# Kernel optimization log

Hardware: AMD Instinct MI355X
Metric: run time of the kernel (lower is better)

The kernel has to match this reference:

```python
import jax, jax.numpy as jnp
import numpy as np
import math

EMBED = 1024
N_HEAD = 16
T_LEN = 2048
BATCH = 2
MLP_MULT = 4
EPS = 1e-5


def setup_inputs() -> dict:
    key = jax.random.key(0)
    ks = jax.random.split(key, 12)
    d = EMBED
    h = MLP_MULT * d
    s = 0.02
    return {
        "x": jax.random.normal(ks[0], (BATCH, T_LEN, d), dtype=jnp.float32),
        "ln1_scale": jnp.ones((d,), jnp.float32),
        "ln1_shift": jnp.zeros((d,), jnp.float32),
        "w_qkv": jax.random.normal(ks[1], (d, 3 * d), jnp.float32) * s,
        "b_qkv": jnp.zeros((3 * d,), jnp.float32),
        "ln2_scale": jnp.ones((d,), jnp.float32),
        "ln2_shift": jnp.zeros((d,), jnp.float32),
        "w_fc": jax.random.normal(ks[2], (d, h), jnp.float32) * s,
        "b_fc": jnp.zeros((h,), jnp.float32),
        "w_proj": jax.random.normal(ks[3], (h, d), jnp.float32) * s,
        "b_proj": jnp.zeros((d,), jnp.float32),
    }


def _layer_norm(x, scale, shift):
    mu = jnp.mean(x, axis=-1, keepdims=True)
    var = jnp.var(x, axis=-1, keepdims=True)
    return (x - mu) * jax.lax.rsqrt(var + EPS) * scale + shift


def _attention(h, w_qkv, b_qkv):
    B, T, C = h.shape
    hd = C // N_HEAD
    qkv = h @ w_qkv + b_qkv  # [B,T,3C]
    q, k, v = jnp.split(qkv, 3, axis=-1)
    q = q.reshape(B, T, N_HEAD, hd)
    k = k.reshape(B, T, N_HEAD, hd)
    v = v.reshape(B, T, N_HEAD, hd)
    scores = jnp.einsum("bthd,bshd->bhts", q, k) * (1.0 / math.sqrt(hd))
    causal = jnp.tril(jnp.ones((T, T), dtype=bool))
    scores = jnp.where(causal[None, None], scores, -jnp.inf)
    probs = jax.nn.softmax(scores, axis=-1)
    y = jnp.einsum("bhts,bshd->bthd", probs, v)
    return y.reshape(B, T, C)


def reference(x, ln1_scale, ln1_shift, w_qkv, b_qkv, ln2_scale, ln2_shift,
              w_fc, b_fc, w_proj, b_proj):
    x = x + _attention(_layer_norm(x, ln1_scale, ln1_shift), w_qkv, b_qkv)
    h = _layer_norm(x, ln2_scale, ln2_shift)
    # note: module names it 'gelu' but it's nn.ReLU()
    h = jax.nn.relu(h @ w_fc + b_fc) @ w_proj + b_proj
    return x + h
```

## Files before the change

### kernel.cpp

```cpp
#include <hip/hip_runtime.h>
#include <hip/hip_bf16.h>


typedef __bf16  bf16x8  __attribute__((ext_vector_type(8)));
typedef __bf16  bf16x4  __attribute__((ext_vector_type(4)));
typedef float   floatx4 __attribute__((ext_vector_type(4)));

#define T_LEN 2048
#define EMB   1024
#define NH    16
#define HD    64
#define HID   4096

#define GLOBAL_LOAD_LDS16(gp, lp) \
    __builtin_amdgcn_global_load_lds( \
        (const __attribute__((address_space(1))) void*)(gp), \
        (__attribute__((address_space(3))) void*)(lp), 16, 0, 0)

__global__ void transpose_cast(const float* __restrict__ in,
                               __bf16* __restrict__ out, int R, int C) {
    __shared__ float tile[32][33];
    int bc = blockIdx.x * 32;
    int br = blockIdx.y * 32;
    int tx = threadIdx.x;
    int ty = threadIdx.y;
    for (int i = 0; i < 32; i += 8) {
        tile[ty + i][tx] = in[(size_t)(br + ty + i) * C + bc + tx];
    }
    __syncthreads();
    for (int i = 0; i < 32; i += 8) {
        int c = bc + ty + i, r = br + tx;
        out[(size_t)c * R + r] = (__bf16)tile[tx][ty + i];
    }
}

__global__ __launch_bounds__(256)
void ln_kernel(const float* __restrict__ in, const float* __restrict__ sc,
               const float* __restrict__ sh, __bf16* __restrict__ out) {
    int row = blockIdx.x;
    const float* p = in + (size_t)row * EMB;
    int tid = threadIdx.x;
    int lane = tid & 63, wave = tid >> 6;
    float v[4];
    float s = 0.f, s2 = 0.f;
    for (int j = 0; j < 4; j++) {
        v[j] = p[tid + j * 256];
        s += v[j]; s2 += v[j] * v[j];
    }
    for (int m = 1; m < 64; m <<= 1) {
        s  += __shfl_xor(s, m);
        s2 += __shfl_xor(s2, m);
    }
    __shared__ float ssum[4], ssum2[4];
    if (lane == 0) { ssum[wave] = s; ssum2[wave] = s2; }
    __syncthreads();
    float tot  = ssum[0] + ssum[1] + ssum[2] + ssum[3];
    float tot2 = ssum2[0] + ssum2[1] + ssum2[2] + ssum2[3];
    float mean = tot * (1.f / EMB);
    float var  = tot2 * (1.f / EMB) - mean * mean;
    float rstd = rsqrtf(var + 1e-5f);
    for (int j = 0; j < 4; j++) {
        int c = tid + j * 256;
        out[(size_t)row * EMB + c] = (__bf16)((v[j] - mean) * rstd * sc[c] + sh[c]);
    }
}

__global__ __launch_bounds__(512)
void gemm256(const __bf16* __restrict__ A, const __bf16* __restrict__ Bt,
             const float* __restrict__ bias, const float* __restrict__ res,
             float* __restrict__ outF, __bf16* __restrict__ outB,
             int M, int N, int lda, int KL, int relu, int gx, int gz) {
    __shared__ __align__(16) __bf16 sA[2][256][64];
    __shared__ __align__(16) __bf16 sB[2][256][64];
    const int BUFE = 256 * 64;
    int tid  = threadIdx.x;
    int lane = tid & 63, wave = tid >> 6;
    int quad = lane >> 4, l16 = lane & 15;

    int i  = blockIdx.x;
    int c  = i & 7, m = i >> 3;
    int bx = m % gx;
    int p  = (m / gx) * 8 + c;
    int by = p / gz;
    int bz = p - by * gz;

    int bm = by * 256, bn = bx * 256;
    size_t k0 = (size_t)bz * KL;
    int wm = (wave >> 2) * 128, wn = (wave & 3) * 64;

    floatx4 acc[8][4] = {};

    int srow  = tid >> 3;
    int sslot = (tid & 7) ^ (srow & 7);
    const __bf16* gA = A  + (size_t)(bm + srow) * lda + k0 + sslot * 8;
    const __bf16* gB = Bt + (size_t)(bn + srow) * lda + k0 + sslot * 8;
    __bf16* lA = &sA[0][0][0] + wave * 512;
    __bf16* lB = &sB[0][0][0] + wave * 512;
    const size_t rstep = (size_t)64 * lda;

#define STAGE256(nb, ko) do { \
    GLOBAL_LOAD_LDS16(gA + (ko),             lA + (nb) * BUFE); \
    GLOBAL_LOAD_LDS16(gB + (ko),             lB + (nb) * BUFE); \
    GLOBAL_LOAD_LDS16(gA + (ko) + rstep,     lA + (nb) * BUFE + 4096); \
    GLOBAL_LOAD_LDS16(gB + (ko) + rstep,     lB + (nb) * BUFE + 4096); \
    GLOBAL_LOAD_LDS16(gA + (ko) + 2 * rstep, lA + (nb) * BUFE + 8192); \
    GLOBAL_LOAD_LDS16(gB + (ko) + 2 * rstep, lB + (nb) * BUFE + 8192); \
    GLOBAL_LOAD_LDS16(gA + (ko) + 3 * rstep, lA + (nb) * BUFE + 12288); \
    GLOBAL_LOAD_LDS16(gB + (ko) + 3 * rstep, lB + (nb) * BUFE + 12288); \
} while (0)

    STAGE256(0, (size_t)0);

    int xs0  = ((quad) ^ (l16 & 7)) * 8;
    int xs1  = ((4 + quad) ^ (l16 & 7)) * 8;
    int aoff = (wm + l16) * 64;
    int boff = (wn + l16) * 64;

    const int nt = KL / 64;
    for (int t = 0; t < nt; ++t) {
        const int cur = t & 1;
        __builtin_amdgcn_s_barrier();
        asm volatile("" ::: "memory");
        if (t + 1 < nt) {
            STAGE256(cur ^ 1, (size_t)(t + 1) * 64);
            asm volatile("s_waitcnt vmcnt(8)" ::: "memory");
        } else {
            asm volatile("s_waitcnt vmcnt(0)" ::: "memory");
        }
        __builtin_amdgcn_s_barrier();
        asm volatile("" ::: "memory");
        __builtin_amdgcn_sched_barrier(0);

        const __bf16* sAc = &sA[0][0][0] + cur * BUFE;
        const __bf16* sBc = &sB[0][0][0] + cur * BUFE;

        bf16x8 a0[4][2], a1[4][2], b0[2][2], b1[2][2];

        #pragma unroll
        for (int mi = 0; mi < 4; ++mi) {
            a0[mi][0] = *(const bf16x8*)(sAc + aoff + mi * 1024 + xs0);
            a0[mi][1] = *(const bf16x8*)(sAc + aoff + mi * 1024 + xs1);
        }
        #pragma unroll
        for (int nj = 0; nj < 2; ++nj) {
            b0[nj][0] = *(const bf16x8*)(sBc + boff + nj * 1024 + xs0);
            b0[nj][1] = *(const bf16x8*)(sBc + boff + nj * 1024 + xs1);
        }
        __builtin_amdgcn_s_setprio(1);
        #pragma unroll
        for (int mi = 0; mi < 4; ++mi)
            #pragma unroll
            for (int nj = 0; nj < 2; ++nj) {
                acc[mi][nj] = __builtin_amdgcn_mfma_f32_16x16x32_bf16(
                    a0[mi][0], b0[nj][0], acc[mi][nj], 0, 0, 0);
                acc[mi][nj] = __builtin_amdgcn_mfma_f32_16x16x32_bf16(
                    a0[mi][1], b0[nj][1], acc[mi][nj], 0, 0, 0);
            }
        __builtin_amdgcn_s_setprio(0);

        #pragma unroll
        for (int nj = 0; nj < 2; ++nj) {
            b1[nj][0] = *(const bf16x8*)(sBc + boff + (2 + nj) * 1024 + xs0);
            b1[nj][1] = *(const bf16x8*)(sBc + boff + (2 + nj) * 1024 + xs1);
        }
        __builtin_amdgcn_s_setprio(1);
        #pragma unroll
        for (int mi = 0; mi < 4; ++mi)
            #pragma unroll
            for (int nj = 0; nj < 2; ++nj) {
                acc[mi][2 + nj] = __builtin_amdgcn_mfma_f32_16x16x32_bf16(
                    a0[mi][0], b1[nj][0], acc[mi][2 + nj], 0, 0, 0);
                acc[mi][2 + nj] = __builtin_amdgcn_mfma_f32_16x16x32_bf16(
                    a0[mi][1], b1[nj][1], acc[mi][2 + nj], 0, 0, 0);
            }
        __builtin_amdgcn_s_setprio(0);

        #pragma unroll
        for (int mi = 0; mi < 4; ++mi) {
            a1[mi][0] = *(const bf16x8*)(sAc + aoff + (4 + mi) * 1024 + xs0);
            a1[mi][1] = *(const bf16x8*)(sAc + aoff + (4 + mi) * 1024 + xs1);
        }
        __builtin_amdgcn_s_setprio(1);
        #pragma unroll
        for (int mi = 0; mi < 4; ++mi)
            #pragma unroll
            for (int nj = 0; nj < 2; ++nj) {
                acc[4 + mi][2 + nj] = __builtin_amdgcn_mfma_f32_16x16x32_bf16(
                    a1[mi][0], b1[nj][0], acc[4 + mi][2 + nj], 0, 0, 0);
                acc[4 + mi][2 + nj] = __builtin_amdgcn_mfma_f32_16x16x32_bf16(
                    a1[mi][1], b1[nj][1], acc[4 + mi][2 + nj], 0, 0, 0);
            }
        __builtin_amdgcn_s_setprio(0);

        __builtin_amdgcn_s_setprio(1);
        #pragma unroll
        for (int mi = 0; mi < 4; ++mi)
            #pragma unroll
            for (int nj = 0; nj < 2; ++nj) {
                acc[4 + mi][nj] = __builtin_amdgcn_mfma_f32_16x16x32_bf16(
                    a1[mi][0], b0[nj][0], acc[4 + mi][nj], 0, 0, 0);
                acc[4 + mi][nj] = __builtin_amdgcn_mfma_f32_16x16x32_bf16(
                    a1[mi][1], b0[nj][1], acc[4 + mi][nj], 0, 0, 0);
            }
        __builtin_amdgcn_s_setprio(0);
    }
#undef STAGE256

    if (bias) {
        #pragma unroll
        for (int mi = 0; mi < 8; ++mi) {
            int row0 = bm + wm + mi * 16 + quad * 4;
            #pragma unroll
            for (int nj = 0; nj < 4; ++nj) {
                int col = bn + wn + nj * 16 + l16;
                float bv = bias[col];
                #pragma unroll
                for (int r = 0; r < 4; ++r) {
                    size_t idx = (size_t)(row0 + r) * N + col;
                    float cc = acc[mi][nj][r] + bv;
                    if (relu) cc = fmaxf(cc, 0.f);
                    if (res)  cc += res[idx];
                    if (outF) outF[idx] = cc;
                    if (outB) outB[idx] = (__bf16)cc;
                }
            }
        }
    } else {
        __bf16* po = outB + (size_t)bz * M * N;
        #pragma unroll
        for (int mi = 0; mi < 8; ++mi) {
            int row0 = bm + wm + mi * 16 + quad * 4;
            #pragma unroll
            for (int nj = 0; nj < 4; ++nj) {
                int col = bn + wn + nj * 16 + l16;
                #pragma unroll
                for (int r = 0; r < 4; ++r)
                    po[(size_t)(row0 + r) * N + col] = (__bf16)acc[mi][nj][r];
            }
        }
    }
}

__global__ __launch_bounds__(256)
void reduce_proj(const __bf16* __restrict__ pbuf, const float* __restrict__ x2,
                 const float* __restrict__ bias, float* __restrict__ out) {
    const size_t MN = (size_t)4096 * 1024;
    size_t i = (size_t)blockIdx.x * 256 + threadIdx.x;
    float4 r = ((const float4*)x2)[i];
    float4 bb = ((const float4*)bias)[i & 255];
    float acc0 = r.x + bb.x, acc1 = r.y + bb.y;
    float acc2 = r.z + bb.z, acc3 = r.w + bb.w;
    for (int k = 0; k < 4; k++) {
        bf16x4 pv = *(const bf16x4*)&pbuf[k * MN + i * 4];
        acc0 += (float)pv[0]; acc1 += (float)pv[1];
        acc2 += (float)pv[2]; acc3 += (float)pv[3];
    }
    float4 o = {acc0, acc1, acc2, acc3};
    ((float4*)out)[i] = o;
}

__global__ __launch_bounds__(256)
void gemm_bt_n64(const __bf16* __restrict__ A, const __bf16* __restrict__ Bt,
                 const float* __restrict__ bias, const float* __restrict__ res,
                 float* __restrict__ outF, __bf16* __restrict__ outB,
                 int M, int N, int K, int relu) {
    __shared__ __align__(16) __bf16 sA[128][40];
    __shared__ __align__(16) __bf16 sB[64][40];
    int tid  = threadIdx.x;
    int lane = tid & 63, wave = tid >> 6;
    int quad = lane >> 4, l16 = lane & 15;
    int bm = blockIdx.y * 128, bn = blockIdx.x * 64;
    int wm = (wave & 1) * 64, wn = (wave >> 1) * 32;
    floatx4 acc[4][2] = {};

    int srow = tid >> 2;
    int scol = (tid & 3) * 8;
    const __bf16* gA = &A[(size_t)(bm + srow) * K + scol];
    const __bf16* gB = &Bt[(size_t)(bn + srow) * K + scol];

    uint4 ra0 = *(const uint4*)gA;
    uint4 ra1 = *(const uint4*)(gA + (size_t)64 * K);
    uint4 rb0 = *(const uint4*)gB;

    for (int kk = 0; kk < K; kk += 32) {
        __syncthreads();
        *(uint4*)&sA[srow][scol]      = ra0;
        *(uint4*)&sA[srow + 64][scol] = ra1;
        *(uint4*)&sB[srow][scol]      = rb0;
        __syncthreads();
        {
            int kn = (kk + 32 < K) ? kk + 32 : kk;
            ra0 = *(const uint4*)(gA + kn);
            ra1 = *(const uint4*)(gA + kn + (size_t)64 * K);
            rb0 = *(const uint4*)(gB + kn);
        }
        bf16x8 af[4], bfr[2];
        for (int i = 0; i < 4; i++)
            af[i] = *(const bf16x8*)&sA[wm + i * 16 + l16][quad * 8];
        for (int j = 0; j < 2; j++)
            bfr[j] = *(const bf16x8*)&sB[wn + j * 16 + l16][quad * 8];
        for (int i = 0; i < 4; i++)
            for (int j = 0; j < 2; j++)
                acc[i][j] = __builtin_amdgcn_mfma_f32_16x16x32_bf16(
                    af[i], bfr[j], acc[i][j], 0, 0, 0);
    }

    for (int i = 0; i < 4; i++) {
        int row0 = bm + wm + i * 16 + quad * 4;
        for (int j = 0; j < 2; j++) {
            int col = bn + wn + j * 16 + l16;
            float bv = bias[col];
            for (int r = 0; r < 4; r++) {
                size_t idx = (size_t)(row0 + r) * N + col;
                float c = acc[i][j][r] + bv;
                if (relu) c = fmaxf(c, 0.f);
                if (res)  c += res[idx];
                if (outF) outF[idx] = c;
                if (outB) outB[idx] = (__bf16)c;
            }
        }
    }
}

__global__ __launch_bounds__(256)
void attn_kernel(const __bf16* __restrict__ qkv, const float* __restrict__ x,
                 float* __restrict__ x2) {
    __shared__ __align__(16) __bf16 sK[2][64][72];
    __shared__ __align__(16) __bf16 sVt[2][64][72];
    __shared__ __align__(16) __bf16 sP[4][16][72];
    const int tid  = threadIdx.x;
    const int lane = tid & 63, wave = tid >> 6;
    const int quad = lane >> 4, l16 = lane & 15;

    int i = blockIdx.x;
    int c = i & 7, m = i >> 3;
    const int bh = (m & 3) * 8 + c;
    const int qb = 31 - (m >> 2);
    const int h  = bh & (NH - 1);
    const int b  = bh >> 4;
    const size_t rowbase = (size_t)b * T_LEN;
    const int qrow = qb * 64 + wave * 16;

    const float kQScale = 0.125f * 1.44269504088896f;
    bf16x8 ones;
    for (int j = 0; j < 8; j++) ones[j] = (__bf16)1.0f;

    const int key0 = tid >> 3, m8 = tid & 7;
    const int key1 = key0 + 32;
    const __bf16* kp0 = qkv + (rowbase + key0) * 3072 + h * HD + m8 * 8 + 1024;
    const __bf16* kp1 = qkv + (rowbase + key1) * 3072 + h * HD + m8 * 8 + 1024;
    const int pc0 = ((key0 >> 3) ^ m8) * 8 + (key0 & 7);
    const int pc1 = ((key1 >> 3) ^ m8) * 8 + (key1 & 7);

    bf16x8 qf[2];
    for (int ks = 0; ks < 2; ks++) {
        bf16x8 raw = *(const bf16x8*)&qkv[(rowbase + qrow + l16) * 3072
                                          + h * HD + ks * 32 + quad * 8];
        for (int j = 0; j < 8; j++)
            qf[ks][j] = (__bf16)((float)raw[j] * kQScale);
    }

    floatx4 o[4] = {}, ol = {};

    const int ntiles = qb + 1;
    const size_t TSTEP = (size_t)64 * 3072;

    uint4 kr0 = *(const uint4*)kp0;
    uint4 kr1 = *(const uint4*)kp1;
    uint4 vr0 = *(const uint4*)(kp0 + 1024);
    uint4 vr1 = *(const uint4*)(kp1 + 1024);
    {
        *(uint4*)&sK[0][key0][m8 * 8] = kr0;
        *(uint4*)&sK[0][key1][m8 * 8] = kr1;
        bf16x8 v0 = *(bf16x8*)&vr0, v1 = *(bf16x8*)&vr1;
        for (int j = 0; j < 8; j++) sVt[0][m8 * 8 + j][pc0] = v0[j];
        for (int j = 0; j < 8; j++) sVt[0][m8 * 8 + j][pc1] = v1[j];
    }
    {
        size_t o1 = (ntiles > 1) ? TSTEP : 0;
        kr0 = *(const uint4*)(kp0 + o1);
        kr1 = *(const uint4*)(kp1 + o1);
        vr0 = *(const uint4*)(kp0 + o1 + 1024);
        vr1 = *(const uint4*)(kp1 + o1 + 1024);
    }
    __syncthreads();

    for (int kt = 0; kt < ntiles; kt++) {
        const int cur = kt & 1, nxt = cur ^ 1;
        if (kt + 1 < ntiles) {
            *(uint4*)&sK[nxt][key0][m8 * 8] = kr0;
            *(uint4*)&sK[nxt][key1][m8 * 8] = kr1;
            bf16x8 v0 = *(bf16x8*)&vr0, v1 = *(bf16x8*)&vr1;
            for (int j = 0; j < 8; j++) sVt[nxt][m8 * 8 + j][pc0] = v0[j];
            for (int j = 0; j < 8; j++) sVt[nxt][m8 * 8 + j][pc1] = v1[j];
            size_t offn = (size_t)((kt + 2 < ntiles) ? kt + 2 : kt + 1) * TSTEP;
            kr0 = *(const uint4*)(kp0 + offn);
            kr1 = *(const uint4*)(kp1 + offn);
            vr0 = *(const uint4*)(kp0 + offn + 1024);
            vr1 = *(const uint4*)(kp1 + offn + 1024);
        }

        floatx4 s_acc[4] = {};
        for (int jt = 0; jt < 4; jt++)
            for (int ks = 0; ks < 2; ks++) {
                bf16x8 kf = *(const bf16x8*)&sK[cur][jt * 16 + l16]
                                              [ks * 32 + quad * 8];
                s_acc[jt] = __builtin_amdgcn_mfma_f32_16x16x32_bf16(
                    qf[ks], kf, s_acc[jt], 0, 0, 0);
            }

        if (kt == qb) {
            const int tq0 = qrow + quad * 4;
            const int k0 = kt * 64;
            for (int jt = 0; jt < 4; jt++) {
                int key = k0 + jt * 16 + l16;
                for (int r = 0; r < 4; r++) {
                    float sv = (key <= tq0 + r) ? s_acc[jt][r] : -1e30f;
                    float pv = __builtin_amdgcn_exp2f(fminf(sv, 30.f));
                    sP[wave][quad * 4 + r][jt * 16 + l16] = (__bf16)pv;
                }
            }
        } else {
            for (int jt = 0; jt < 4; jt++)
                for (int r = 0; r < 4; r++) {
                    float pv = __builtin_amdgcn_exp2f(fminf(s_acc[jt][r], 30.f));
                    sP[wave][quad * 4 + r][jt * 16 + l16] = (__bf16)pv;
                }
        }

        for (int kp = 0; kp < 2; kp++) {
            bf16x8 pf = *(const bf16x8*)&sP[wave][l16][kp * 32 + quad * 8];
            ol = __builtin_amdgcn_mfma_f32_16x16x32_bf16(pf, ones, ol, 0, 0, 0);
            for (int jt2 = 0; jt2 < 4; jt2++) {
                int d = jt2 * 16 + l16;
                int pg = (kp * 4 + quad) ^ (d >> 3);
                bf16x8 vf = *(const bf16x8*)&sVt[cur][d][pg * 8];
                o[jt2] = __builtin_amdgcn_mfma_f32_16x16x32_bf16(
                    pf, vf, o[jt2], 0, 0, 0);
            }
        }
        __syncthreads();
    }

    float inv[4];
    for (int r = 0; r < 4; r++) inv[r] = __builtin_amdgcn_rcpf(ol[r]);
    for (int jt2 = 0; jt2 < 4; jt2++) {
        for (int r = 0; r < 4; r++) {
            int tq  = qrow + quad * 4 + r;
            int col = h * HD + jt2 * 16 + l16;
            size_t gi = (rowbase + tq) * EMB + col;
            x2[gi] = x[gi] + o[jt2][r] * inv[r];
        }
    }
}

extern "C" void kernel_launch(void* const* d_in, const int* in_sizes, int n_in,
                              void* d_out, int out_size, void* d_ws, size_t ws_size,
                              hipStream_t stream) {
    const float* x      = (const float*)d_in[0];
    const float* ln1_s  = (const float*)d_in[1];
    const float* ln1_b  = (const float*)d_in[2];
    const float* w_qkv  = (const float*)d_in[3];
    const float* b_qkv  = (const float*)d_in[4];
    const float* ln2_s  = (const float*)d_in[5];
    const float* ln2_b  = (const float*)d_in[6];
    const float* w_fc   = (const float*)d_in[7];
    const float* b_fc   = (const float*)d_in[8];
    const float* w_proj = (const float*)d_in[9];
    const float* b_proj = (const float*)d_in[10];
    float* out = (float*)d_out;

    const int M = 2 * T_LEN;
    char* ws = (char*)d_ws;
    size_t off = 0;
    auto alloc = [&](size_t bytes) {
        void* p = ws + off; off += (bytes + 255) & ~(size_t)255; return p;
    };
    __bf16* wpj_t  = (__bf16*)alloc((size_t)1024 * 4096 * 2);
    float*  x2     = (float*) alloc((size_t)M * 1024 * 4);
    __bf16* hfc    = (__bf16*)alloc((size_t)M * 4096 * 2);
    size_t mark = off;
    __bf16* wqkv_t = (__bf16*)alloc((size_t)3072 * 1024 * 2);
    __bf16* wfc_t  = (__bf16*)alloc((size_t)4096 * 1024 * 2);
    __bf16* h1     = (__bf16*)alloc((size_t)M * 1024 * 2);
    __bf16* h2     = (__bf16*)alloc((size_t)M * 1024 * 2);
    __bf16* qkvb   = (__bf16*)alloc((size_t)M * 3072 * 2);
    __bf16* pbuf = (__bf16*)(ws + mark);
    size_t need = mark + (size_t)4 * M * 1024 * 2;
    bool can_split = ws_size >= need;

    dim3 tb(32, 8);
    transpose_cast<<<dim3(3072 / 32, 1024 / 32), tb, 0, stream>>>(w_qkv, wqkv_t, 1024, 3072);
    transpose_cast<<<dim3(4096 / 32, 1024 / 32), tb, 0, stream>>>(w_fc,  wfc_t,  1024, 4096);
    transpose_cast<<<dim3(1024 / 32, 4096 / 32), tb, 0, stream>>>(w_proj, wpj_t, 4096, 1024);

    ln_kernel<<<M, 256, 0, stream>>>(x, ln1_s, ln1_b, h1);

    gemm256<<<192, 512, 0, stream>>>(
        h1, wqkv_t, b_qkv, nullptr, nullptr, qkvb, M, 3072, 1024, 1024, 0,
        12, 1);

    attn_kernel<<<1024, 256, 0, stream>>>(qkvb, x, x2);

    ln_kernel<<<M, 256, 0, stream>>>(x2, ln2_s, ln2_b, h2);

    gemm256<<<256, 512, 0, stream>>>(
        h2, wfc_t, b_fc, nullptr, nullptr, hfc, M, 4096, 1024, 1024, 1,
        16, 1);

    if (can_split) {
        gemm256<<<256, 512, 0, stream>>>(
            hfc, wpj_t, nullptr, nullptr, nullptr, pbuf, M, 1024, 4096, 1024, 0,
            4, 4);
        reduce_proj<<<(M * 1024 / 4) / 256, 256, 0, stream>>>(
            pbuf, x2, b_proj, out);
    } else {
        gemm_bt_n64<<<dim3(1024 / 64, M / 128), 256, 0, stream>>>(
            hfc, wpj_t, b_proj, x2, out, nullptr, M, 1024, 4096, 0);
    }
}
```

Baseline: 303.7 us.

## Split QK^T across waves by key slice and share P via swizzled LDS

In the attention kernel, each wave now computes scores for all 64 query rows against its own 16-key slice. Previously each wave computed its own 16 query rows against all 64 keys. Each K fragment is read from LDS once and reused across four query tiles, and the probabilities are written to a shared, XOR-swizzled 64x64 P buffer. An extra barrier per tile is needed before the PV step, and Q fragments for all four query tiles are held in registers, which raises register pressure. The GEMM inner MFMA loops are also reordered so the k-slice is the outer loop, giving more independent accumulators back to back.

```diff
diff --git a/kernel.cpp b/kernel.cpp
--- a/kernel.cpp
+++ b/kernel.cpp
@@ -148,14 +148,13 @@
         }
         __builtin_amdgcn_s_setprio(1);
         #pragma unroll
-        for (int mi = 0; mi < 4; ++mi)
+        for (int ks = 0; ks < 2; ++ks)
             #pragma unroll
-            for (int nj = 0; nj < 2; ++nj) {
-                acc[mi][nj] = __builtin_amdgcn_mfma_f32_16x16x32_bf16(
-                    a0[mi][0], b0[nj][0], acc[mi][nj], 0, 0, 0);
-                acc[mi][nj] = __builtin_amdgcn_mfma_f32_16x16x32_bf16(
-                    a0[mi][1], b0[nj][1], acc[mi][nj], 0, 0, 0);
-            }
+            for (int mi = 0; mi < 4; ++mi)
+                #pragma unroll
+                for (int nj = 0; nj < 2; ++nj)
+                    acc[mi][nj] = __builtin_amdgcn_mfma_f32_16x16x32_bf16(
+                        a0[mi][ks], b0[nj][ks], acc[mi][nj], 0, 0, 0);
         __builtin_amdgcn_s_setprio(0);
 
         #pragma unroll
@@ -165,14 +164,13 @@
         }
         __builtin_amdgcn_s_setprio(1);
         #pragma unroll
-        for (int mi = 0; mi < 4; ++mi)
+        for (int ks = 0; ks < 2; ++ks)
             #pragma unroll
-            for (int nj = 0; nj < 2; ++nj) {
-                acc[mi][2 + nj] = __builtin_amdgcn_mfma_f32_16x16x32_bf16(
-                    a0[mi][0], b1[nj][0], acc[mi][2 + nj], 0, 0, 0);
-                acc[mi][2 + nj] = __builtin_amdgcn_mfma_f32_16x16x32_bf16(
-                    a0[mi][1], b1[nj][1], acc[mi][2 + nj], 0, 0, 0);
-            }
+            for (int mi = 0; mi < 4; ++mi)
+                #pragma unroll
+                for (int nj = 0; nj < 2; ++nj)
+                    acc[mi][2 + nj] = __builtin_amdgcn_mfma_f32_16x16x32_bf16(
+                        a0[mi][ks], b1[nj][ks], acc[mi][2 + nj], 0, 0, 0);
         __builtin_amdgcn_s_setprio(0);
 
         #pragma unroll
@@ -182,26 +180,24 @@
         }
         __builtin_amdgcn_s_setprio(1);
         #pragma unroll
-        for (int mi = 0; mi < 4; ++mi)
+        for (int ks = 0; ks < 2; ++ks)
             #pragma unroll
-            for (int nj = 0; nj < 2; ++nj) {
-                acc[4 + mi][2 + nj] = __builtin_amdgcn_mfma_f32_16x16x32_bf16(
-                    a1[mi][0], b1[nj][0], acc[4 + mi][2 + nj], 0, 0, 0);
-                acc[4 + mi][2 + nj] = __builtin_amdgcn_mfma_f32_16x16x32_bf16(
-                    a1[mi][1], b1[nj][1], acc[4 + mi][2 + nj], 0, 0, 0);
-            }
+            for (int mi = 0; mi < 4; ++mi)
+                #pragma unroll
+                for (int nj = 0; nj < 2; ++nj)
+                    acc[4 + mi][2 + nj] = __builtin_amdgcn_mfma_f32_16x16x32_bf16(
+                        a1[mi][ks], b1[nj][ks], acc[4 + mi][2 + nj], 0, 0, 0);
         __builtin_amdgcn_s_setprio(0);
 
         __builtin_amdgcn_s_setprio(1);
         #pragma unroll
-        for (int mi = 0; mi < 4; ++mi)
+        for (int ks = 0; ks < 2; ++ks)
             #pragma unroll
-            for (int nj = 0; nj < 2; ++nj) {
-                acc[4 + mi][nj] = __builtin_amdgcn_mfma_f32_16x16x32_bf16(
-                    a1[mi][0], b0[nj][0], acc[4 + mi][nj], 0, 0, 0);
-                acc[4 + mi][nj] = __builtin_amdgcn_mfma_f32_16x16x32_bf16(
-                    a1[mi][1], b0[nj][1], acc[4 + mi][nj], 0, 0, 0);
-            }
+            for (int mi = 0; mi < 4; ++mi)
+                #pragma unroll
+                for (int nj = 0; nj < 2; ++nj)
+                    acc[4 + mi][nj] = __builtin_amdgcn_mfma_f32_16x16x32_bf16(
+                        a1[mi][ks], b0[nj][ks], acc[4 + mi][nj], 0, 0, 0);
         __builtin_amdgcn_s_setprio(0);
     }
 #undef STAGE256
@@ -327,7 +323,7 @@
                  float* __restrict__ x2) {
     __shared__ __align__(16) __bf16 sK[2][64][72];
     __shared__ __align__(16) __bf16 sVt[2][64][72];
-    __shared__ __align__(16) __bf16 sP[4][16][72];
+    __shared__ __align__(16) __bf16 sP[64][64];
     const int tid  = threadIdx.x;
     const int lane = tid & 63, wave = tid >> 6;
     const int quad = lane >> 4, l16 = lane & 15;
@@ -352,13 +348,14 @@
     const int pc0 = ((key0 >> 3) ^ m8) * 8 + (key0 & 7);
     const int pc1 = ((key1 >> 3) ^ m8) * 8 + (key1 & 7);
 
-    bf16x8 qf[2];
-    for (int ks = 0; ks < 2; ks++) {
-        bf16x8 raw = *(const bf16x8*)&qkv[(rowbase + qrow + l16) * 3072
-                                          + h * HD + ks * 32 + quad * 8];
-        for (int j = 0; j < 8; j++)
-            qf[ks][j] = (__bf16)((float)raw[j] * kQScale);
-    }
+    bf16x8 qf[4][2];
+    for (int qi = 0; qi < 4; qi++)
+        for (int ks = 0; ks < 2; ks++) {
+            bf16x8 raw = *(const bf16x8*)&qkv[(rowbase + qb * 64 + qi * 16 + l16)
+                                              * 3072 + h * HD + ks * 32 + quad * 8];
+            for (int j = 0; j < 8; j++)
+                qf[qi][ks][j] = (__bf16)((float)raw[j] * kQScale);
+        }
 
     floatx4 o[4] = {}, ol = {};
 
@@ -401,35 +398,39 @@
         }
 
         floatx4 s_acc[4] = {};
-        for (int jt = 0; jt < 4; jt++)
-            for (int ks = 0; ks < 2; ks++) {
-                bf16x8 kf = *(const bf16x8*)&sK[cur][jt * 16 + l16]
-                                              [ks * 32 + quad * 8];
-                s_acc[jt] = __builtin_amdgcn_mfma_f32_16x16x32_bf16(
-                    qf[ks], kf, s_acc[jt], 0, 0, 0);
-            }
-
+        for (int ks = 0; ks < 2; ks++) {
+            bf16x8 kf = *(const bf16x8*)&sK[cur][wave * 16 + l16]
+                                          [ks * 32 + quad * 8];
+            for (int qi = 0; qi < 4; qi++)
+                s_acc[qi] = __builtin_amdgcn_mfma_f32_16x16x32_bf16(
+                    qf[qi][ks], kf, s_acc[qi], 0, 0, 0);
+        }
+
+        const int kk = wave * 16 + l16;
         if (kt == qb) {
-            const int tq0 = qrow + quad * 4;
-            const int k0 = kt * 64;
-            for (int jt = 0; jt < 4; jt++) {
-                int key = k0 + jt * 16 + l16;
+            for (int qi = 0; qi < 4; qi++)
                 for (int r = 0; r < 4; r++) {
-                    float sv = (key <= tq0 + r) ? s_acc[jt][r] : -1e30f;
+                    int tq = qi * 16 + quad * 4 + r;
+                    float sv = (kk <= tq) ? s_acc[qi][r] : -1e30f;
                     float pv = __builtin_amdgcn_exp2f(fminf(sv, 30.f));
-                    sP[wave][quad * 4 + r][jt * 16 + l16] = (__bf16)pv;
+                    sP[tq][kk ^ ((quad * 2 + (r >> 1)) << 3)] = (__bf16)pv;
                 }
-            }
         } else {
-            for (int jt = 0; jt < 4; jt++)
+            for (int qi = 0; qi < 4; qi++)
                 for (int r = 0; r < 4; r++) {
-                    float pv = __builtin_amdgcn_exp2f(fminf(s_acc[jt][r], 30.f));
-                    sP[wave][quad * 4 + r][jt * 16 + l16] = (__bf16)pv;
+                    float pv = __builtin_amdgcn_exp2f(fminf(s_acc[qi][r], 30.f));
+                    sP[qi * 16 + quad * 4 + r]
+                      [kk ^ ((quad * 2 + (r >> 1)) << 3)] = (__bf16)pv;
                 }
         }
 
+        asm volatile("s_waitcnt lgkmcnt(0)" ::: "memory");
+        __builtin_amdgcn_s_barrier();
+        asm volatile("" ::: "memory");
+
         for (int kp = 0; kp < 2; kp++) {
-            bf16x8 pf = *(const bf16x8*)&sP[wave][l16][kp * 32 + quad * 8];
+            bf16x8 pf = *(const bf16x8*)&sP[wave * 16 + l16]
+                          [(kp * 32 + quad * 8) ^ ((l16 >> 1) << 3)];
             ol = __builtin_amdgcn_mfma_f32_16x16x32_bf16(pf, ones, ol, 0, 0, 0);
             for (int jt2 = 0; jt2 < 4; jt2++) {
                 int d = jt2 * 16 + l16;
```

After: 309.1 us. About the same (+1.8%).

## Process 128 query rows per attention block and reorder GEMM MFMA k-loop

Applied to the files above, without the earlier changes.

The attention kernel now uses 512-thread blocks that cover 128 query rows (8 waves) instead of 64. Each K/V tile staged in shared memory is reused by twice as many query waves, which halves global K/V traffic and the number of blocks. The cost is that the lower-half waves sit idle on the last diagonal tile, and the larger blocks may lower occupancy. Separately, the GEMM inner MFMA loops are reordered so that the k-slice is the outer loop, which spaces out dependent accumulations into the same accumulator.

```diff
diff --git a/kernel.cpp b/kernel.cpp
--- a/kernel.cpp
+++ b/kernel.cpp
@@ -148,14 +148,13 @@
         }
         __builtin_amdgcn_s_setprio(1);
         #pragma unroll
-        for (int mi = 0; mi < 4; ++mi)
+        for (int ks = 0; ks < 2; ++ks)
             #pragma unroll
-            for (int nj = 0; nj < 2; ++nj) {
-                acc[mi][nj] = __builtin_amdgcn_mfma_f32_16x16x32_bf16(
-                    a0[mi][0], b0[nj][0], acc[mi][nj], 0, 0, 0);
-                acc[mi][nj] = __builtin_amdgcn_mfma_f32_16x16x32_bf16(
-                    a0[mi][1], b0[nj][1], acc[mi][nj], 0, 0, 0);
-            }
+            for (int mi = 0; mi < 4; ++mi)
+                #pragma unroll
+                for (int nj = 0; nj < 2; ++nj)
+                    acc[mi][nj] = __builtin_amdgcn_mfma_f32_16x16x32_bf16(
+                        a0[mi][ks], b0[nj][ks], acc[mi][nj], 0, 0, 0);
         __builtin_amdgcn_s_setprio(0);
 
         #pragma unroll
@@ -165,14 +164,13 @@
         }
         __builtin_amdgcn_s_setprio(1);
         #pragma unroll
-        for (int mi = 0; mi < 4; ++mi)
+        for (int ks = 0; ks < 2; ++ks)
             #pragma unroll
-            for (int nj = 0; nj < 2; ++nj) {
-                acc[mi][2 + nj] = __builtin_amdgcn_mfma_f32_16x16x32_bf16(
-                    a0[mi][0], b1[nj][0], acc[mi][2 + nj], 0, 0, 0);
-                acc[mi][2 + nj] = __builtin_amdgcn_mfma_f32_16x16x32_bf16(
-                    a0[mi][1], b1[nj][1], acc[mi][2 + nj], 0, 0, 0);
-            }
+            for (int mi = 0; mi < 4; ++mi)
+                #pragma unroll
+                for (int nj = 0; nj < 2; ++nj)
+                    acc[mi][2 + nj] = __builtin_amdgcn_mfma_f32_16x16x32_bf16(
+                        a0[mi][ks], b1[nj][ks], acc[mi][2 + nj], 0, 0, 0);
         __builtin_amdgcn_s_setprio(0);
 
         #pragma unroll
@@ -182,26 +180,24 @@
         }
         __builtin_amdgcn_s_setprio(1);
         #pragma unroll
-        for (int mi = 0; mi < 4; ++mi)
+        for (int ks = 0; ks < 2; ++ks)
             #pragma unroll
-            for (int nj = 0; nj < 2; ++nj) {
-                acc[4 + mi][2 + nj] = __builtin_amdgcn_mfma_f32_16x16x32_bf16(
-                    a1[mi][0], b1[nj][0], acc[4 + mi][2 + nj], 0, 0, 0);
-                acc[4 + mi][2 + nj] = __builtin_amdgcn_mfma_f32_16x16x32_bf16(
-                    a1[mi][1], b1[nj][1], acc[4 + mi][2 + nj], 0, 0, 0);
-            }
+            for (int mi = 0; mi < 4; ++mi)
+                #pragma unroll
+                for (int nj = 0; nj < 2; ++nj)
+                    acc[4 + mi][2 + nj] = __builtin_amdgcn_mfma_f32_16x16x32_bf16(
+                        a1[mi][ks], b1[nj][ks], acc[4 + mi][2 + nj], 0, 0, 0);
         __builtin_amdgcn_s_setprio(0);
 
         __builtin_amdgcn_s_setprio(1);
         #pragma unroll
-        for (int mi = 0; mi < 4; ++mi)
+        for (int ks = 0; ks < 2; ++ks)
             #pragma unroll
-            for (int nj = 0; nj < 2; ++nj) {
-                acc[4 + mi][nj] = __builtin_amdgcn_mfma_f32_16x16x32_bf16(
-                    a1[mi][0], b0[nj][0], acc[4 + mi][nj], 0, 0, 0);
-                acc[4 + mi][nj] = __builtin_amdgcn_mfma_f32_16x16x32_bf16(
-                    a1[mi][1], b0[nj][1], acc[4 + mi][nj], 0, 0, 0);
-            }
+            for (int mi = 0; mi < 4; ++mi)
+                #pragma unroll
+                for (int nj = 0; nj < 2; ++nj)
+                    acc[4 + mi][nj] = __builtin_amdgcn_mfma_f32_16x16x32_bf16(
+                        a1[mi][ks], b0[nj][ks], acc[4 + mi][nj], 0, 0, 0);
         __builtin_amdgcn_s_setprio(0);
     }
 #undef STAGE256
@@ -322,35 +318,33 @@
     }
 }
 
-__global__ __launch_bounds__(256)
+__global__ __launch_bounds__(512)
 void attn_kernel(const __bf16* __restrict__ qkv, const float* __restrict__ x,
                  float* __restrict__ x2) {
     __shared__ __align__(16) __bf16 sK[2][64][72];
     __shared__ __align__(16) __bf16 sVt[2][64][72];
-    __shared__ __align__(16) __bf16 sP[4][16][72];
+    __shared__ __align__(16) __bf16 sP[8][16][72];
     const int tid  = threadIdx.x;
     const int lane = tid & 63, wave = tid >> 6;
     const int quad = lane >> 4, l16 = lane & 15;
 
     int i = blockIdx.x;
     int c = i & 7, m = i >> 3;
-    const int bh = (m & 3) * 8 + c;
-    const int qb = 31 - (m >> 2);
-    const int h  = bh & (NH - 1);
-    const int b  = bh >> 4;
+    const int bh  = (m & 3) * 8 + c;
+    const int qbp = 15 - (m >> 2);
+    const int h   = bh & (NH - 1);
+    const int b   = bh >> 4;
     const size_t rowbase = (size_t)b * T_LEN;
-    const int qrow = qb * 64 + wave * 16;
+    const int qrow = qbp * 128 + wave * 16;
+    const int dt   = 2 * qbp + (wave >> 2);
 
     const float kQScale = 0.125f * 1.44269504088896f;
     bf16x8 ones;
     for (int j = 0; j < 8; j++) ones[j] = (__bf16)1.0f;
 
     const int key0 = tid >> 3, m8 = tid & 7;
-    const int key1 = key0 + 32;
     const __bf16* kp0 = qkv + (rowbase + key0) * 3072 + h * HD + m8 * 8 + 1024;
-    const __bf16* kp1 = qkv + (rowbase + key1) * 3072 + h * HD + m8 * 8 + 1024;
     const int pc0 = ((key0 >> 3) ^ m8) * 8 + (key0 & 7);
-    const int pc1 = ((key1 >> 3) ^ m8) * 8 + (key1 & 7);
 
     bf16x8 qf[2];
     for (int ks = 0; ks < 2; ks++) {
@@ -362,81 +356,70 @@
 
     floatx4 o[4] = {}, ol = {};
 
-    const int ntiles = qb + 1;
+    const int ntiles = 2 * qbp + 2;
     const size_t TSTEP = (size_t)64 * 3072;
 
     uint4 kr0 = *(const uint4*)kp0;
-    uint4 kr1 = *(const uint4*)kp1;
     uint4 vr0 = *(const uint4*)(kp0 + 1024);
-    uint4 vr1 = *(const uint4*)(kp1 + 1024);
     {
         *(uint4*)&sK[0][key0][m8 * 8] = kr0;
-        *(uint4*)&sK[0][key1][m8 * 8] = kr1;
-        bf16x8 v0 = *(bf16x8*)&vr0, v1 = *(bf16x8*)&vr1;
+        bf16x8 v0 = *(bf16x8*)&vr0;
         for (int j = 0; j < 8; j++) sVt[0][m8 * 8 + j][pc0] = v0[j];
-        for (int j = 0; j < 8; j++) sVt[0][m8 * 8 + j][pc1] = v1[j];
-    }
-    {
-        size_t o1 = (ntiles > 1) ? TSTEP : 0;
-        kr0 = *(const uint4*)(kp0 + o1);
-        kr1 = *(const uint4*)(kp1 + o1);
-        vr0 = *(const uint4*)(kp0 + o1 + 1024);
-        vr1 = *(const uint4*)(kp1 + o1 + 1024);
-    }
+    }
+    kr0 = *(const uint4*)(kp0 + TSTEP);
+    vr0 = *(const uint4*)(kp0 + TSTEP + 1024);
     __syncthreads();
 
     for (int kt = 0; kt < ntiles; kt++) {
         const int cur = kt & 1, nxt = cur ^ 1;
         if (kt + 1 < ntiles) {
             *(uint4*)&sK[nxt][key0][m8 * 8] = kr0;
-            *(uint4*)&sK[nxt][key1][m8 * 8] = kr1;
-            bf16x8 v0 = *(bf16x8*)&vr0, v1 = *(bf16x8*)&vr1;
+            bf16x8 v0 = *(bf16x8*)&vr0;
             for (int j = 0; j < 8; j++) sVt[nxt][m8 * 8 + j][pc0] = v0[j];
-            for (int j = 0; j < 8; j++) sVt[nxt][m8 * 8 + j][pc1] = v1[j];
             size_t offn = (size_t)((kt + 2 < ntiles) ? kt + 2 : kt + 1) * TSTEP;
             kr0 = *(const uint4*)(kp0 + offn);
-            kr1 = *(const uint4*)(kp1 + offn);
             vr0 = *(const uint4*)(kp0 + offn + 1024);
-            vr1 = *(const uint4*)(kp1 + offn + 1024);
-        }
-
-        floatx4 s_acc[4] = {};
-        for (int jt = 0; jt < 4; jt++)
-            for (int ks = 0; ks < 2; ks++) {
-                bf16x8 kf = *(const bf16x8*)&sK[cur][jt * 16 + l16]
-                                              [ks * 32 + quad * 8];
-                s_acc[jt] = __builtin_amdgcn_mfma_f32_16x16x32_bf16(
-                    qf[ks], kf, s_acc[jt], 0, 0, 0);
+        }
+
+        if (kt <= dt) {
+            floatx4 s_acc[4] = {};
+            for (int jt = 0; jt < 4; jt++)
+                for (int ks = 0; ks < 2; ks++) {
+                    bf16x8 kf = *(const bf16x8*)&sK[cur][jt * 16 + l16]
+                                                  [ks * 32 + quad * 8];
+                    s_acc[jt] = __builtin_amdgcn_mfma_f32_16x16x32_bf16(
+                        qf[ks], kf, s_acc[jt], 0, 0, 0);
+                }
+
+            if (kt == dt) {
+                const int tq0 = qrow + quad * 4;
+                const int k0 = kt * 64;
+                for (int jt = 0; jt < 4; jt++) {
+                    int key = k0 + jt * 16 + l16;
+                    for (int r = 0; r < 4; r++) {
+                        float sv = (key <= tq0 + r) ? s_acc[jt][r] : -1e30f;
+                        float pv = __builtin_amdgcn_exp2f(fminf(sv, 30.f));
+                        sP[wave][quad * 4 + r][jt * 16 + l16] = (__bf16)pv;
+                    }
+                }
+            } else {
+                for (int jt = 0; jt < 4; jt++)
+                    for (int r = 0; r < 4; r++) {
+                        float pv = __builtin_amdgcn_exp2f(fminf(s_acc[jt][r], 30.f));
+                        sP[wave][quad * 4 + r][jt * 16 + l16] = (__bf16)pv;
+                    }
             }
 
-        if (kt == qb) {
-            const int tq0 = qrow + quad * 4;
-            const int k0 = kt * 64;
-            for (int jt = 0; jt < 4; jt++) {
-                int key = k0 + jt * 16 + l16;
-                for (int r = 0; r < 4; r++) {
-                    float sv = (key <= tq0 + r) ? s_acc[jt][r] : -1e30f;
-                    float pv = __builtin_amdgcn_exp2f(fminf(sv, 30.f));
-                    sP[wave][quad * 4 + r][jt * 16 + l16] = (__bf16)pv;
+            for (int kp = 0; kp < 2; kp++) {
+                bf16x8 pf = *(const bf16x8*)&sP[wave][l16][kp * 32 + quad * 8];
+                ol = __builtin_amdgcn_mfma_f32_16x16x32_bf16(pf, ones, ol, 0, 0, 0);
+                for (int jt2 = 0; jt2 < 4; jt2++) {
+                    int d = jt2 * 16 + l16;
+                    int pg = (kp * 4 + quad) ^ (d >> 3);
+                    bf16x8 vf = *(const bf16x8*)&sVt[cur][d][pg * 8];
+                    o[jt2] = __builtin_amdgcn_mfma_f32_16x16x32_bf16(
+                        pf, vf, o[jt2], 0, 0, 0);
                 }
-            }
-        } else {
-            for (int jt = 0; jt < 4; jt++)
-                for (int r = 0; r < 4; r++) {
-                    float pv = __builtin_amdgcn_exp2f(fminf(s_acc[jt][r], 30.f));
-                    sP[wave][quad * 4 + r][jt * 16 + l16] = (__bf16)pv;
-                }
-        }
-
-        for (int kp = 0; kp < 2; kp++) {
-            bf16x8 pf = *(const bf16x8*)&sP[wave][l16][kp * 32 + quad * 8];
-            ol = __builtin_amdgcn_mfma_f32_16x16x32_bf16(pf, ones, ol, 0, 0, 0);
-            for (int jt2 = 0; jt2 < 4; jt2++) {
-                int d = jt2 * 16 + l16;
-                int pg = (kp * 4 + quad) ^ (d >> 3);
-                bf16x8 vf = *(const bf16x8*)&sVt[cur][d][pg * 8];
-                o[jt2] = __builtin_amdgcn_mfma_f32_16x16x32_bf16(
-                    pf, vf, o[jt2], 0, 0, 0);
             }
         }
         __syncthreads();
@@ -500,7 +483,7 @@
         h1, wqkv_t, b_qkv, nullptr, nullptr, qkvb, M, 3072, 1024, 1024, 0,
         12, 1);
 
-    attn_kernel<<<1024, 256, 0, stream>>>(qkvb, x, x2);
+    attn_kernel<<<512, 512, 0, stream>>>(qkvb, x, x2);
 
     ln_kernel<<<M, 256, 0, stream>>>(x2, ln2_s, ln2_b, h2);
 
```

Measured after the change: 304.4 us. Within noise of the previous version (+0.2%).
